# Performance work log

Hardware: AMD Instinct MI355X
Metric: run time of the kernel (lower is better)

Reference implementation:

```python
import jax, jax.numpy as jnp
import numpy as np
from jax import lax

B, N, C, W, D = 128, 16384, 8, 10, 3   # batch, input_size, n_channels, out_window, poly_degree
L = N - W + 1                          # in-filter tap length
EPS = 1e-5


def setup_inputs() -> dict:
    key = jax.random.key(0)
    ks = jax.random.split(key, 8)
    x = jax.random.normal(ks[0], (B, N, C, 2), dtype=jnp.float32)
    # torch Linear-style scale ~ 1/sqrt(fan_in)
    w_in_real = jax.random.normal(ks[1], (C, L), dtype=jnp.float32) * (L ** -0.5)
    w_in_imag = jax.random.normal(ks[2], (C, L), dtype=jnp.float32) * (L ** -0.5)
    fan_coeff = 2 * (C - 1) * D
    w_coeff = jax.random.normal(ks[3], (C, 2, fan_coeff), dtype=jnp.float32) * (fan_coeff ** -0.5)
    w_out_real = jax.random.normal(ks[4], (C, W), dtype=jnp.float32) * (W ** -0.5)
    w_out_imag = jax.random.normal(ks[5], (C, W), dtype=jnp.float32) * (W ** -0.5)
    bn_gamma = jnp.ones((C,), dtype=jnp.float32)
    bn_beta = jnp.zeros((C,), dtype=jnp.float32)
    return {"x": x, "w_in_real": w_in_real, "w_in_imag": w_in_imag,
            "w_coeff": w_coeff, "w_out_real": w_out_real,
            "w_out_imag": w_out_imag, "bn_gamma": bn_gamma, "bn_beta": bn_beta}


# complement index map: row c lists all channels != c
_IDX = np.array([[j for j in range(C) if j != c] for c in range(C)])  # (C, C-1)


def _grouped_fir(sig, w):
    # sig: (B, N, C); per-channel length-L correlation -> (B, W, C)
    out = lax.conv_general_dilated(
        jnp.transpose(sig, (0, 2, 1)),      # (B, C, N)
        w[:, None, :],                      # (C, 1, L)
        window_strides=(1,), padding='VALID', feature_group_count=C)
    return jnp.transpose(out, (0, 2, 1))    # (B, W, C)


def reference(x, w_in_real, w_in_imag, w_coeff, w_out_real, w_out_imag, bn_gamma, bn_beta):
    fr = _grouped_fir(x[..., 0], w_in_real)   # (B, W, C)
    fi = _grouped_fir(x[..., 1], w_in_imag)   # (B, W, C)

    # polynomial expansion: pow_d = fr^d + fi^d, d = 1..D
    powd = jnp.stack([fr ** d + fi ** d for d in range(1, D + 1)], axis=-1)  # (B, W, C, D)
    poly_r = powd * fr[..., None]
    poly_i = powd * fi[..., None]

    # cross-channel coeff layers: input layout = [real(all j != c), imag(all j != c)]
    rg = poly_r[:, :, _IDX, :]                      # (B, W, C, C-1, D)
    ig = poly_i[:, :, _IDX, :]
    Wc = w_coeff.reshape(C, 2, 2, C - 1, D)         # (c, out, real/imag half, j, d)
    nonlin = (jnp.einsum('bwcjd,cpjd->bwcp', rg, Wc[:, :, 0]) +
              jnp.einsum('bwcjd,cpjd->bwcp', ig, Wc[:, :, 1]))  # (B, W, C, 2)

    out_r = jnp.einsum('bwc,cw->bc', nonlin[..., 0], w_out_real)
    out_i = jnp.einsum('bwc,cw->bc', nonlin[..., 1], w_out_imag)
    out = jnp.stack([out_r, out_i], axis=-1)        # (B, C, 2)

    # BatchNorm1d over (batch, last) per channel, training-mode batch stats
    mean = out.mean(axis=(0, 2), keepdims=True)
    var = out.var(axis=(0, 2), keepdims=True)
    return (out - mean) / jnp.sqrt(var + EPS) * bn_gamma[None, :, None] + bn_beta[None, :, None]
```

## Files before the change

### kernel.cpp

```cpp
#include <hip/hip_runtime.h>

#define BB 128
#define NN 16384
#define CC 8
#define WW 10
#define DD 3
#define LL 16375
#define LP 16392
#define SEG 8
#define CHUNKS 32
#define CHLEN 64
#define BPB 16
#define ABLK (BB / BPB)

__global__ __launch_bounds__(256) void k_interleave(const float* __restrict__ wr,
                                                    const float* __restrict__ wi,
                                                    float* __restrict__ w2) {
  int idx = blockIdx.x * 256 + threadIdx.x;
  if (idx >= LP * CC) return;
  int l = idx >> 3;
  int c = idx & 7;
  float a = 0.f, b = 0.f;
  if (l < LL) { a = wr[c * LL + l]; b = wi[c * LL + l]; }
  w2[2 * idx]     = a;
  w2[2 * idx + 1] = b;
}

__global__ __launch_bounds__(256) void k_fir(const float* __restrict__ x,
                                             const float* __restrict__ w2,
                                             float* __restrict__ fpart) {
  int b   = blockIdx.x >> 3;
  int seg = blockIdx.x & 7;
  int tid = threadIdx.x;
  int c     = tid & 7;
  int chunk = tid >> 3;
  int n0 = seg * (NN / SEG) + chunk * CHLEN;

  const float2* __restrict__ xp  = ((const float2*)x)  + (size_t)b * NN * CC + c;
  const float2* __restrict__ wpt = ((const float2*)w2) + c;

  float2 acc[WW];
#pragma unroll
  for (int w = 0; w < WW; ++w) { acc[w].x = 0.f; acc[w].y = 0.f; }

  float2 ww[16];
#pragma unroll
  for (int s = 0; s < 16; ++s) { ww[s].x = 0.f; ww[s].y = 0.f; }
#pragma unroll
  for (int j = 1; j <= 9; ++j) {
    int l = n0 - j;
    if (l >= 0) ww[(16 - j) & 15] = wpt[(size_t)l * CC];
  }

  for (int g = 0; g < CHLEN / 16; ++g) {
    int nb = n0 + g * 16;
#pragma unroll
    for (int u = 0; u < 16; ++u) {
      int n = nb + u;
      ww[u] = wpt[(size_t)n * CC];
      float2 xv = xp[(size_t)n * CC];
#pragma unroll
      for (int w = 0; w < WW; ++w) {
        float2 wt = ww[(u - w + 16) & 15];
        acc[w].x += xv.x * wt.x;
        acc[w].y += xv.y * wt.y;
      }
    }
  }

  __shared__ float red[256 * 20];
#pragma unroll
  for (int w = 0; w < WW; ++w) {
    red[tid * 20 + 2 * w]     = acc[w].x;
    red[tid * 20 + 2 * w + 1] = acc[w].y;
  }
  __syncthreads();
  if (tid < 160) {
    int cc = (tid >> 1) & 7;
    int wv = tid >> 4;
    int ri = tid & 1;
    int k  = 2 * wv + ri;
    float s = 0.f;
    for (int ch = 0; ch < 32; ++ch) s += red[(ch * 8 + cc) * 20 + k];
    fpart[(size_t)blockIdx.x * 160 + tid] = s;
  }
}

__global__ __launch_bounds__(256) void k_nonlin(const float* __restrict__ fpart,
                                                const float* __restrict__ wc,
                                                const float* __restrict__ wor,
                                                const float* __restrict__ woi,
                                                float* __restrict__ oraw,
                                                float* __restrict__ part) {
  __shared__ float sred[BPB][164];
  __shared__ float swc[704];
  __shared__ float swout[160];

  int tid = threadIdx.x;
  int blk = blockIdx.x;
  int b0 = blk * BPB;

  for (int i = tid; i < 672; i += 256) swc[i] = wc[i];
  if (tid < 80) swout[tid] = wor[tid];
  else if (tid < 160) swout[tid] = woi[tid - 80];

  {
    const float4* fp4 = (const float4*)fpart;
    for (int o4 = tid; o4 < BPB * 40; o4 += 256) {
      int bl = o4 / 40;
      int r4 = o4 - bl * 40;
      float4 s = {0.f, 0.f, 0.f, 0.f};
      size_t base = ((size_t)(b0 + bl) * 8) * 40 + r4;
#pragma unroll
      for (int seg = 0; seg < 8; ++seg) {
        float4 v = fp4[base + (size_t)seg * 40];
        s.x += v.x; s.y += v.y; s.z += v.z; s.w += v.w;
      }
      int r = r4 * 4;
      sred[bl][r] = s.x; sred[bl][r + 1] = s.y; sred[bl][r + 2] = s.z; sred[bl][r + 3] = s.w;
    }
  }
  __syncthreads();

  int b = tid >> 4;
  int c = (tid >> 1) & 7;
  int p = tid & 1;

  float wreg[8][2][3];
#pragma unroll
  for (int j = 0; j < 8; ++j) {
    int jj = j - (j > c ? 1 : 0);
    if (j == c) jj = 0;
#pragma unroll
    for (int ri = 0; ri < 2; ++ri)
#pragma unroll
      for (int d = 0; d < 3; ++d) {
        float v = swc[(c * 2 + p) * 42 + ri * 21 + jj * 3 + d];
        wreg[j][ri][d] = (j == c) ? 0.f : v;
      }
  }

  float o = 0.f;
  const float* wop = swout + p * 80 + c * 10;
#pragma unroll
  for (int w = 0; w < WW; ++w) {
    float4 f0 = *(const float4*)&sred[b][w * 16];
    float4 f1 = *(const float4*)&sred[b][w * 16 + 4];
    float4 f2 = *(const float4*)&sred[b][w * 16 + 8];
    float4 f3 = *(const float4*)&sred[b][w * 16 + 12];
    float fv[16] = {f0.x, f0.y, f0.z, f0.w, f1.x, f1.y, f1.z, f1.w,
                    f2.x, f2.y, f2.z, f2.w, f3.x, f3.y, f3.z, f3.w};
    float nl0 = 0.f, nl1 = 0.f, nl2 = 0.f;
#pragma unroll
    for (int j = 0; j < 8; ++j) {
      float r  = fv[2 * j];
      float im = fv[2 * j + 1];
      float r2 = r * r, i2 = im * im;
      float pw0 = r + im;
      float pw1 = r2 + i2;
      float pw2 = r2 * r + i2 * im;
      nl0 += (pw0 * r) * wreg[j][0][0] + (pw0 * im) * wreg[j][1][0];
      nl1 += (pw1 * r) * wreg[j][0][1] + (pw1 * im) * wreg[j][1][1];
      nl2 += (pw2 * r) * wreg[j][0][2] + (pw2 * im) * wreg[j][1][2];
    }
    o += (nl0 + nl1 + nl2) * wop[w];
  }

  oraw[((size_t)(b0 + b) * CC + c) * 2 + p] = o;

  __shared__ float sval[256], ssq[256];
  sval[tid] = o;
  ssq[tid]  = o * o;
  __syncthreads();
  if (tid < 8) {
    float S = 0.f, Q = 0.f;
#pragma unroll
    for (int k = 0; k < 32; ++k) {
      int t = (k >> 1) * 16 + tid * 2 + (k & 1);
      S += sval[t];
      Q += ssq[t];
    }
    part[(blk * 8 + tid) * 2 + 0] = S;
    part[(blk * 8 + tid) * 2 + 1] = Q;
  }
}

__global__ __launch_bounds__(256) void k_bn(const float* __restrict__ oraw,
                                            const float* __restrict__ part,
                                            const float* __restrict__ gamma,
                                            const float* __restrict__ beta,
                                            float* __restrict__ out) {
  __shared__ float mv[8], iv[8], bv[8];
  int tid = threadIdx.x;
  if (tid < 8) {
    float S = 0.f, Q = 0.f;
#pragma unroll
    for (int blk = 0; blk < ABLK; ++blk) {
      S += part[(blk * 8 + tid) * 2 + 0];
      Q += part[(blk * 8 + tid) * 2 + 1];
    }
    float mean = S * (1.0f / 256.0f);
    float var  = Q * (1.0f / 256.0f) - mean * mean;
    mv[tid] = mean;
    iv[tid] = gamma[tid] * rsqrtf(var + 1e-5f);
    bv[tid] = beta[tid];
  }
  __syncthreads();
  for (int i = tid; i < BB * CC * 2; i += 256) {
    int c = (i >> 1) & 7;
    out[i] = (oraw[i] - mv[c]) * iv[c] + bv[c];
  }
}

extern "C" void kernel_launch(void* const* d_in, const int* in_sizes, int n_in,
                              void* d_out, int out_size, void* d_ws, size_t ws_size,
                              hipStream_t stream) {
  const float* x   = (const float*)d_in[0];
  const float* wr  = (const float*)d_in[1];
  const float* wi  = (const float*)d_in[2];
  const float* wc  = (const float*)d_in[3];
  const float* wor = (const float*)d_in[4];
  const float* woi = (const float*)d_in[5];
  const float* gm  = (const float*)d_in[6];
  const float* bt  = (const float*)d_in[7];
  float* out = (float*)d_out;

  float* ws    = (float*)d_ws;
  float* w2    = ws;
  float* fpart = w2 + (size_t)CC * LP * 2;
  float* oraw  = fpart + (size_t)BB * SEG * 160;
  float* part  = oraw + BB * CC * 2;

  k_interleave<<<dim3((LP * CC + 255) / 256), dim3(256), 0, stream>>>(wr, wi, w2);
  k_fir<<<dim3(BB * SEG), dim3(256), 0, stream>>>(x, w2, fpart);
  k_nonlin<<<dim3(ABLK), dim3(256), 0, stream>>>(fpart, wc, wor, woi, oraw, part);
  k_bn<<<dim3(1), dim3(256), 0, stream>>>(oraw, part, gm, bt, out);
}
```

Before: 46.47 us.

## Process two batches per FIR block and fuse nonlinear and BatchNorm kernels

The FIR kernel now handles two batch rows per block with 512 threads. Each loaded weight tap is reused across both batches, and x is read with nontemporal loads. The cross-chunk reduction uses wave shuffles instead of a large shared-memory array. The nonlinear stage and BatchNorm are fused into a single 1024-thread, single-block kernel that processes the batch in two halves, removing one launch and the oraw/part round trips at the cost of running on a single CU.

```diff
diff --git a/kernel.cpp b/kernel.cpp
--- a/kernel.cpp
+++ b/kernel.cpp
@@ -8,10 +8,10 @@
 #define LL 16375
 #define LP 16392
 #define SEG 8
-#define CHUNKS 32
-#define CHLEN 64
-#define BPB 16
-#define ABLK (BB / BPB)
+#define CHLEN 32
+#define BP 2
+
+typedef float f2_t __attribute__((ext_vector_type(2)));
 
 __global__ __launch_bounds__(256) void k_interleave(const float* __restrict__ wr,
                                                     const float* __restrict__ wi,
@@ -26,26 +26,28 @@
   w2[2 * idx + 1] = b;
 }
 
-__global__ __launch_bounds__(256) void k_fir(const float* __restrict__ x,
-                                             const float* __restrict__ w2,
-                                             float* __restrict__ fpart) {
-  int b   = blockIdx.x >> 3;
+__global__ __launch_bounds__(512, 4) void k_fir(const float* __restrict__ x,
+                                                const float* __restrict__ w2,
+                                                float* __restrict__ fpart) {
+  int bp  = blockIdx.x >> 3;
   int seg = blockIdx.x & 7;
+  int b0  = bp * BP;
   int tid = threadIdx.x;
   int c     = tid & 7;
   int chunk = tid >> 3;
   int n0 = seg * (NN / SEG) + chunk * CHLEN;
 
-  const float2* __restrict__ xp  = ((const float2*)x)  + (size_t)b * NN * CC + c;
-  const float2* __restrict__ wpt = ((const float2*)w2) + c;
-
-  float2 acc[WW];
-#pragma unroll
-  for (int w = 0; w < WW; ++w) { acc[w].x = 0.f; acc[w].y = 0.f; }
-
-  float2 ww[16];
-#pragma unroll
-  for (int s = 0; s < 16; ++s) { ww[s].x = 0.f; ww[s].y = 0.f; }
+  const f2_t* __restrict__ xpA = ((const f2_t*)x) + (size_t)(b0)     * NN * CC + c;
+  const f2_t* __restrict__ xpB = ((const f2_t*)x) + (size_t)(b0 + 1) * NN * CC + c;
+  const f2_t* __restrict__ wpt = ((const f2_t*)w2) + c;
+
+  f2_t accA[WW], accB[WW];
+#pragma unroll
+  for (int w = 0; w < WW; ++w) { accA[w] = (f2_t)0.f; accB[w] = (f2_t)0.f; }
+
+  f2_t ww[16];
+#pragma unroll
+  for (int s = 0; s < 16; ++s) ww[s] = (f2_t)0.f;
 #pragma unroll
   for (int j = 1; j <= 9; ++j) {
     int l = n0 - j;
@@ -58,73 +60,91 @@
     for (int u = 0; u < 16; ++u) {
       int n = nb + u;
       ww[u] = wpt[(size_t)n * CC];
-      float2 xv = xp[(size_t)n * CC];
+      f2_t xa = __builtin_nontemporal_load(&xpA[(size_t)n * CC]);
+      f2_t xb = __builtin_nontemporal_load(&xpB[(size_t)n * CC]);
 #pragma unroll
       for (int w = 0; w < WW; ++w) {
-        float2 wt = ww[(u - w + 16) & 15];
-        acc[w].x += xv.x * wt.x;
-        acc[w].y += xv.y * wt.y;
-      }
-    }
-  }
-
-  __shared__ float red[256 * 20];
-#pragma unroll
-  for (int w = 0; w < WW; ++w) {
-    red[tid * 20 + 2 * w]     = acc[w].x;
-    red[tid * 20 + 2 * w + 1] = acc[w].y;
-  }
-  __syncthreads();
-  if (tid < 160) {
-    int cc = (tid >> 1) & 7;
-    int wv = tid >> 4;
-    int ri = tid & 1;
-    int k  = 2 * wv + ri;
+        f2_t wt = ww[(u - w + 16) & 15];
+        accA[w][0] += xa[0] * wt[0];
+        accA[w][1] += xa[1] * wt[1];
+        accB[w][0] += xb[0] * wt[0];
+        accB[w][1] += xb[1] * wt[1];
+      }
+    }
+  }
+
+#pragma unroll
+  for (int m = 8; m < 64; m <<= 1) {
+#pragma unroll
+    for (int w = 0; w < WW; ++w) {
+      accA[w][0] += __shfl_xor(accA[w][0], m);
+      accA[w][1] += __shfl_xor(accA[w][1], m);
+      accB[w][0] += __shfl_xor(accB[w][0], m);
+      accB[w][1] += __shfl_xor(accB[w][1], m);
+    }
+  }
+
+  __shared__ float red[8 * 320];
+  int wave = tid >> 6;
+  int lane = tid & 63;
+  if (lane < 8) {
+#pragma unroll
+    for (int w = 0; w < WW; ++w) {
+      red[wave * 320 +       w * 16 + lane * 2 + 0] = accA[w][0];
+      red[wave * 320 +       w * 16 + lane * 2 + 1] = accA[w][1];
+      red[wave * 320 + 160 + w * 16 + lane * 2 + 0] = accB[w][0];
+      red[wave * 320 + 160 + w * 16 + lane * 2 + 1] = accB[w][1];
+    }
+  }
+  __syncthreads();
+  if (tid < 320) {
     float s = 0.f;
-    for (int ch = 0; ch < 32; ++ch) s += red[(ch * 8 + cc) * 20 + k];
-    fpart[(size_t)blockIdx.x * 160 + tid] = s;
-  }
-}
-
-__global__ __launch_bounds__(256) void k_nonlin(const float* __restrict__ fpart,
+#pragma unroll
+    for (int wv = 0; wv < 8; ++wv) s += red[wv * 320 + tid];
+    int bi = tid >> 7 >> 1;
+    bi = (tid >= 160) ? 1 : 0;
+    int r = tid - bi * 160;
+    fpart[((size_t)(b0 + bi) * SEG + seg) * 160 + r] = s;
+  }
+}
+
+__global__ __launch_bounds__(1024) void k_final(const float* __restrict__ fpart,
                                                 const float* __restrict__ wc,
                                                 const float* __restrict__ wor,
                                                 const float* __restrict__ woi,
-                                                float* __restrict__ oraw,
-                                                float* __restrict__ part) {
-  __shared__ float sred[BPB][164];
-  __shared__ float swc[704];
+                                                const float* __restrict__ gamma,
+                                                const float* __restrict__ beta,
+                                                float* __restrict__ out) {
+  __shared__ float sred[64][164];
+  __shared__ float swc[672];
   __shared__ float swout[160];
+  __shared__ float ps[16][8], qs[16][8];
+  __shared__ float mv[8], iv[8], bv[8];
 
   int tid = threadIdx.x;
-  int blk = blockIdx.x;
-  int b0 = blk * BPB;
-
-  for (int i = tid; i < 672; i += 256) swc[i] = wc[i];
-  if (tid < 80) swout[tid] = wor[tid];
-  else if (tid < 160) swout[tid] = woi[tid - 80];
-
-  {
-    const float4* fp4 = (const float4*)fpart;
-    for (int o4 = tid; o4 < BPB * 40; o4 += 256) {
-      int bl = o4 / 40;
-      int r4 = o4 - bl * 40;
-      float4 s = {0.f, 0.f, 0.f, 0.f};
-      size_t base = ((size_t)(b0 + bl) * 8) * 40 + r4;
-#pragma unroll
-      for (int seg = 0; seg < 8; ++seg) {
-        float4 v = fp4[base + (size_t)seg * 40];
-        s.x += v.x; s.y += v.y; s.z += v.z; s.w += v.w;
-      }
-      int r = r4 * 4;
-      sred[bl][r] = s.x; sred[bl][r + 1] = s.y; sred[bl][r + 2] = s.z; sred[bl][r + 3] = s.w;
-    }
-  }
-  __syncthreads();
-
-  int b = tid >> 4;
-  int c = (tid >> 1) & 7;
-  int p = tid & 1;
+  if (tid < 672) swc[tid] = wc[tid];
+  if (tid >= 768 && tid < 848) swout[tid - 768] = wor[tid - 768];
+  if (tid >= 848 && tid < 928) swout[tid - 768] = woi[tid - 848];
+
+  int b2 = tid >> 4;
+  int c  = (tid >> 1) & 7;
+  int p  = tid & 1;
+
+  const float4* fp4 = (const float4*)fpart;
+
+  for (int t = tid; t < 64 * 40; t += 1024) {
+    int bl = t / 40;
+    int r4 = t - bl * 40;
+    float4 s = {0.f, 0.f, 0.f, 0.f};
+    size_t base = ((size_t)bl * SEG) * 40 + r4;
+#pragma unroll
+    for (int seg = 0; seg < SEG; ++seg) {
+      float4 v = fp4[base + (size_t)seg * 40];
+      s.x += v.x; s.y += v.y; s.z += v.z; s.w += v.w;
+    }
+    *(float4*)&sred[bl][r4 * 4] = s;
+  }
+  __syncthreads();
 
   float wreg[8][2][3];
 #pragma unroll
@@ -139,66 +159,68 @@
         wreg[j][ri][d] = (j == c) ? 0.f : v;
       }
   }
-
-  float o = 0.f;
   const float* wop = swout + p * 80 + c * 10;
-#pragma unroll
-  for (int w = 0; w < WW; ++w) {
-    float4 f0 = *(const float4*)&sred[b][w * 16];
-    float4 f1 = *(const float4*)&sred[b][w * 16 + 4];
-    float4 f2 = *(const float4*)&sred[b][w * 16 + 8];
-    float4 f3 = *(const float4*)&sred[b][w * 16 + 12];
-    float fv[16] = {f0.x, f0.y, f0.z, f0.w, f1.x, f1.y, f1.z, f1.w,
-                    f2.x, f2.y, f2.z, f2.w, f3.x, f3.y, f3.z, f3.w};
-    float nl0 = 0.f, nl1 = 0.f, nl2 = 0.f;
-#pragma unroll
-    for (int j = 0; j < 8; ++j) {
-      float r  = fv[2 * j];
-      float im = fv[2 * j + 1];
-      float r2 = r * r, i2 = im * im;
-      float pw0 = r + im;
-      float pw1 = r2 + i2;
-      float pw2 = r2 * r + i2 * im;
-      nl0 += (pw0 * r) * wreg[j][0][0] + (pw0 * im) * wreg[j][1][0];
-      nl1 += (pw1 * r) * wreg[j][0][1] + (pw1 * im) * wreg[j][1][1];
-      nl2 += (pw2 * r) * wreg[j][0][2] + (pw2 * im) * wreg[j][1][2];
-    }
-    o += (nl0 + nl1 + nl2) * wop[w];
-  }
-
-  oraw[((size_t)(b0 + b) * CC + c) * 2 + p] = o;
-
-  __shared__ float sval[256], ssq[256];
-  sval[tid] = o;
-  ssq[tid]  = o * o;
+
+  float o0, o1;
+#pragma unroll
+  for (int half = 0; half < 2; ++half) {
+    float o = 0.f;
+#pragma unroll
+    for (int w = 0; w < WW; ++w) {
+      float4 f0 = *(const float4*)&sred[b2][w * 16];
+      float4 f1 = *(const float4*)&sred[b2][w * 16 + 4];
+      float4 f2 = *(const float4*)&sred[b2][w * 16 + 8];
+      float4 f3 = *(const float4*)&sred[b2][w * 16 + 12];
+      float fv[16] = {f0.x, f0.y, f0.z, f0.w, f1.x, f1.y, f1.z, f1.w,
+                      f2.x, f2.y, f2.z, f2.w, f3.x, f3.y, f3.z, f3.w};
+      float nl0 = 0.f, nl1 = 0.f, nl2 = 0.f;
+#pragma unroll
+      for (int j = 0; j < 8; ++j) {
+        float r  = fv[2 * j];
+        float im = fv[2 * j + 1];
+        float r2 = r * r, i2 = im * im;
+        float pw0 = r + im;
+        float pw1 = r2 + i2;
+        float pw2 = r2 * r + i2 * im;
+        nl0 += (pw0 * r) * wreg[j][0][0] + (pw0 * im) * wreg[j][1][0];
+        nl1 += (pw1 * r) * wreg[j][0][1] + (pw1 * im) * wreg[j][1][1];
+        nl2 += (pw2 * r) * wreg[j][0][2] + (pw2 * im) * wreg[j][1][2];
+      }
+      o += (nl0 + nl1 + nl2) * wop[w];
+    }
+    if (half == 0) {
+      o0 = o;
+      __syncthreads();
+      for (int t = tid; t < 64 * 40; t += 1024) {
+        int bl = t / 40;
+        int r4 = t - bl * 40;
+        float4 s = {0.f, 0.f, 0.f, 0.f};
+        size_t base = ((size_t)(64 + bl) * SEG) * 40 + r4;
+#pragma unroll
+        for (int seg = 0; seg < SEG; ++seg) {
+          float4 v = fp4[base + (size_t)seg * 40];
+          s.x += v.x; s.y += v.y; s.z += v.z; s.w += v.w;
+        }
+        *(float4*)&sred[bl][r4 * 4] = s;
+      }
+      __syncthreads();
+    } else {
+      o1 = o;
+    }
+  }
+
+  float s  = o0 + o1;
+  float sq = o0 * o0 + o1 * o1;
+  s  += __shfl_xor(s, 1);   sq += __shfl_xor(sq, 1);
+  s  += __shfl_xor(s, 16);  sq += __shfl_xor(sq, 16);
+  s  += __shfl_xor(s, 32);  sq += __shfl_xor(sq, 32);
+  int wave = tid >> 6, lane = tid & 63;
+  if ((lane & 0x31) == 0) { ps[wave][(lane >> 1) & 7] = s; qs[wave][(lane >> 1) & 7] = sq; }
   __syncthreads();
   if (tid < 8) {
     float S = 0.f, Q = 0.f;
 #pragma unroll
-    for (int k = 0; k < 32; ++k) {
-      int t = (k >> 1) * 16 + tid * 2 + (k & 1);
-      S += sval[t];
-      Q += ssq[t];
-    }
-    part[(blk * 8 + tid) * 2 + 0] = S;
-    part[(blk * 8 + tid) * 2 + 1] = Q;
-  }
-}
-
-__global__ __launch_bounds__(256) void k_bn(const float* __restrict__ oraw,
-                                            const float* __restrict__ part,
-                                            const float* __restrict__ gamma,
-                                            const float* __restrict__ beta,
-                                            float* __restrict__ out) {
-  __shared__ float mv[8], iv[8], bv[8];
-  int tid = threadIdx.x;
-  if (tid < 8) {
-    float S = 0.f, Q = 0.f;
-#pragma unroll
-    for (int blk = 0; blk < ABLK; ++blk) {
-      S += part[(blk * 8 + tid) * 2 + 0];
-      Q += part[(blk * 8 + tid) * 2 + 1];
-    }
+    for (int k = 0; k < 16; ++k) { S += ps[k][tid]; Q += qs[k][tid]; }
     float mean = S * (1.0f / 256.0f);
     float var  = Q * (1.0f / 256.0f) - mean * mean;
     mv[tid] = mean;
@@ -206,10 +228,9 @@
     bv[tid] = beta[tid];
   }
   __syncthreads();
-  for (int i = tid; i < BB * CC * 2; i += 256) {
-    int c = (i >> 1) & 7;
-    out[i] = (oraw[i] - mv[c]) * iv[c] + bv[c];
-  }
+
+  out[tid]        = (o0 - mv[c]) * iv[c] + bv[c];
+  out[tid + 1024] = (o1 - mv[c]) * iv[c] + bv[c];
 }
 
 extern "C" void kernel_launch(void* const* d_in, const int* in_sizes, int n_in,
@@ -228,11 +249,8 @@
   float* ws    = (float*)d_ws;
   float* w2    = ws;
   float* fpart = w2 + (size_t)CC * LP * 2;
-  float* oraw  = fpart + (size_t)BB * SEG * 160;
-  float* part  = oraw + BB * CC * 2;
 
   k_interleave<<<dim3((LP * CC + 255) / 256), dim3(256), 0, stream>>>(wr, wi, w2);
-  k_fir<<<dim3(BB * SEG), dim3(256), 0, stream>>>(x, w2, fpart);
-  k_nonlin<<<dim3(ABLK), dim3(256), 0, stream>>>(fpart, wc, wor, woi, oraw, part);
-  k_bn<<<dim3(1), dim3(256), 0, stream>>>(oraw, part, gm, bt, out);
-}
+  k_fir<<<dim3((BB / BP) * SEG), dim3(512), 0, stream>>>(x, w2, fpart);
+  k_final<<<dim3(1), dim3(1024), 0, stream>>>(fpart, wc, wor, woi, gm, bt, out);
+}
```

Result: slower. 86.63 us (+86.4%).
